# Performance work log

Measured on AMD Instinct MI355X. Metric: run time of the kernel, lower is better.

## Reference

```python
import jax, jax.numpy as jnp
import numpy as np

D_MODEL = 256

def setup_inputs() -> dict:
    key = jax.random.key(0)
    k_x, k_wqkv, k_bqkv, k_wp, k_bp = jax.random.split(key, 5)
    B, T, d = 4, 4096, D_MODEL
    bound_qkv = 1.0 / np.sqrt(d)
    return {
        "x": jax.random.normal(k_x, (B, T, d), dtype=jnp.float32),
        "W_qkv": jax.random.uniform(k_wqkv, (d, 3 * d), jnp.float32, -bound_qkv, bound_qkv),
        "b_qkv": jax.random.uniform(k_bqkv, (3 * d,), jnp.float32, -bound_qkv, bound_qkv),
        "W_proj": jax.random.uniform(k_wp, (d, d), jnp.float32, -bound_qkv, bound_qkv),
        "b_proj": jax.random.uniform(k_bp, (d,), jnp.float32, -bound_qkv, bound_qkv),
    }

def reference(x, W_qkv, b_qkv, W_proj, b_proj):
    B, T, d = x.shape
    qkv = x @ W_qkv + b_qkv                       # (B, T, 3d)
    q, k, v = jnp.split(qkv, 3, axis=-1)          # each (B, T, d)
    scale = 1.0 / np.sqrt(d).astype(np.float32)
    scores = jnp.einsum('btd,bsd->bts', q, k) * scale   # (B, T, T)
    causal = jnp.tril(jnp.ones((T, T), dtype=bool))     # allowed positions
    scores = jnp.where(causal, scores, -jnp.inf)
    weights = jax.nn.softmax(scores, axis=-1)           # (B, T, T)
    ctx = jnp.einsum('bts,bsd->btd', weights, v)        # (B, T, d)
    return ctx @ W_proj + b_proj
```

## Files before the change

### kernel.cpp

```cpp
#include <hip/hip_runtime.h>
#include <math.h>

#define TT 4096
#define BB 4
#define DM 256
#define NSEG_B 144

typedef __attribute__((ext_vector_type(8))) short short8;
typedef __attribute__((ext_vector_type(4))) short short4v;
typedef __attribute__((ext_vector_type(4))) float f32x4;

#define MFMA16(a, b, c) __builtin_amdgcn_mfma_f32_16x16x32_bf16(a, b, c, 0, 0, 0)

#define GL2LDS(gp, lp) __builtin_amdgcn_global_load_lds( \
    (const __attribute__((address_space(1))) unsigned int*)(gp), \
    (__attribute__((address_space(3))) unsigned int*)(lp), 16, 0, 0)

__device__ __forceinline__ short f2b(float f) {
    union { float f; unsigned u; } v; v.f = f;
    unsigned r = v.u + 0x7FFFu + ((v.u >> 16) & 1u);
    return (short)(r >> 16);
}

__global__ __launch_bounds__(256) void transpose_cast2(
    const float* __restrict__ W1, short* __restrict__ Wt1,
    const float* __restrict__ W2, short* __restrict__ Wt2)
{
    __shared__ float T[64 * 68];
    const int tid = threadIdx.x;
    const int by = blockIdx.y;
    const float* W; short* Wt; int N, n0;
    if (by < 12) { W = W1; Wt = Wt1; N = 768; n0 = by * 64; }
    else         { W = W2; Wt = Wt2; N = 256; n0 = (by - 12) * 64; }
    const int k0 = blockIdx.x * 64;
#pragma unroll
    for (int it = 0; it < 4; ++it) {
        int idx = tid + it * 256;
        int r = idx >> 4, c4 = idx & 15;
        *(float4*)&T[r * 68 + c4 * 4] =
            *(const float4*)&W[(size_t)(k0 + r) * N + n0 + c4 * 4];
    }
    __syncthreads();
#pragma unroll
    for (int it = 0; it < 4; ++it) {
        int idx = tid + it * 256;
        int n = idx >> 4, c4 = idx & 15;
        short4v t;
#pragma unroll
        for (int j = 0; j < 4; ++j) t[j] = f2b(T[(c4 * 4 + j) * 68 + n]);
        *(short4v*)&Wt[(size_t)(n0 + n) * 256 + k0 + c4 * 4] = t;
    }
}

__global__ __launch_bounds__(256) void qkv_gemm(
    const float* __restrict__ x, const short* __restrict__ Bt,
    const float* __restrict__ bias, short* __restrict__ qkvb,
    short* __restrict__ VtG)
{
    __shared__ short As[16384];
    __shared__ short Bs[16384];
    __shared__ short Ts[64 * 72];

    const int tid = threadIdx.x;
    const int w = tid >> 6, lane = tid & 63;
    const int l15 = lane & 15, quad = lane >> 4;
    const int m0 = blockIdx.x * 64;
    const int nsup = blockIdx.y * 384;

#pragma unroll
    for (int it = 0; it < 8; ++it) {
        int idx = tid + it * 256;
        int row = ((idx >> 9) << 4) + (idx & 15);
        int col = ((idx >> 6) & 7) * 32 + ((idx >> 4) & 3) * 8;
        const float* src = &x[(size_t)(m0 + row) * 256 + col];
        float4 u = *(const float4*)src, u2 = *(const float4*)(src + 4);
        short8 t;
        t[0] = f2b(u.x);  t[1] = f2b(u.y);  t[2] = f2b(u.z);  t[3] = f2b(u.w);
        t[4] = f2b(u2.x); t[5] = f2b(u2.y); t[6] = f2b(u2.z); t[7] = f2b(u2.w);
        *(short8*)&As[idx * 8] = t;
    }

    for (int t6 = 0; t6 < 6; ++t6) {
        const int n0 = nsup + t6 * 64;
#pragma unroll
        for (int it = 0; it < 8; ++it) {
            int idx = tid + it * 256;
            int n = ((idx >> 9) << 4) + (idx & 15);
            int col = ((idx >> 6) & 7) * 32 + ((idx >> 4) & 3) * 8;
            *(short8*)&Bs[idx * 8] = *(const short8*)&Bt[(size_t)(n0 + n) * 256 + col];
        }
        __syncthreads();

        f32x4 acc[4];
#pragma unroll
        for (int t = 0; t < 4; ++t) acc[t] = (f32x4){0.f, 0.f, 0.f, 0.f};
#pragma unroll
        for (int k0 = 0; k0 < 8; ++k0) {
            short8 a = *(const short8*)&As[((w * 8 + k0) * 64 + lane) * 8];
#pragma unroll
            for (int nt = 0; nt < 4; ++nt) {
                short8 bb = *(const short8*)&Bs[((nt * 8 + k0) * 64 + lane) * 8];
                acc[nt] = MFMA16(a, bb, acc[nt]);
            }
        }

        if (n0 < 512) {
#pragma unroll
            for (int nt = 0; nt < 4; ++nt) {
                int n = n0 + nt * 16 + l15;
                float bv = bias[n];
#pragma unroll
                for (int r = 0; r < 4; ++r)
                    qkvb[(size_t)(m0 + w * 16 + quad * 4 + r) * 768 + n]
                        = f2b(acc[nt][r] + bv);
            }
            __syncthreads();
        } else {
#pragma unroll
            for (int nt = 0; nt < 4; ++nt) {
                int n = n0 + nt * 16 + l15;
                float bv = bias[n];
#pragma unroll
                for (int r = 0; r < 4; ++r)
                    Ts[(nt * 16 + l15) * 72 + w * 16 + quad * 4 + r]
                        = f2b(acc[nt][r] + bv);
            }
            __syncthreads();
            const int d  = tid >> 2;
            const int c  = tid & 3;
            short8 v0 = *(const short8*)&Ts[d * 72 + c * 16];
            short8 v1 = *(const short8*)&Ts[d * 72 + c * 16 + 8];
            const int bg = m0 >> 12, key0 = (m0 & 4095) + c * 16;
            short* dst = &VtG[((size_t)bg * 256 + (n0 - 512) + d) * 4096 + key0];
            *(short8*)dst = v0;
            *(short8*)(dst + 8) = v1;
        }
    }
}

__global__ __launch_bounds__(256, 2) void flash_mfma(
    const short* __restrict__ qkv,
    const short* __restrict__ VtG,
    float* __restrict__ Opart,
    float* __restrict__ L)
{
    __shared__ short Ks[2][8192];
    __shared__ short Vs[2][8192];
    __shared__ short Ps[4096];

    const int tid = threadIdx.x;
    const int w = tid >> 6, lane = tid & 63;
    const int l15 = lane & 15, quad = lane >> 4;

    const int b = blockIdx.x & 3;
    const int e = (NSEG_B - 1) - (blockIdx.x >> 2);
    const int lid = b * NSEG_B + e;
    int g = 0;
    while (g < 7 && e >= 2 * (g + 1) * (g + 2)) ++g;
    int off = e - 2 * g * (g + 1);
    int qt = 4 * g + off / (g + 1);
    int s  = off - (off / (g + 1)) * (g + 1);
    const int kb_lo = s * 16;
    const int kb_hi = min(kb_lo + 16, 4 * (qt + 1));
    const int nunits = kb_hi - kb_lo;

    const size_t base = (size_t)b * TT * 768;
    const int row0 = qt * 128;

    short8 aq[2][8];
#pragma unroll
    for (int rs = 0; rs < 2; ++rs) {
        const short* qrow = &qkv[base + (size_t)(row0 + rs * 64 + w * 16 + l15) * 768 + quad * 8];
#pragma unroll
        for (int k0 = 0; k0 < 8; ++k0)
            aq[rs][k0] = *(const short8*)&qrow[k0 * 32];
    }

#pragma unroll
    for (int it = 0; it < 4; ++it) {
        int idx = tid + it * 256;
        int row = ((idx >> 9) << 4) + (idx & 15);
        int col = ((idx >> 6) & 7) * 32 + ((idx >> 4) & 3) * 8;
        GL2LDS(&qkv[base + (size_t)(kb_lo * 32 + row) * 768 + 256 + col], &Ks[0][idx * 8]);
        int d  = ((idx >> 6) << 4) + (idx & 15);
        int kc = ((idx >> 4) & 3) * 8;
        GL2LDS(&VtG[((size_t)b * 256 + d) * 4096 + kb_lo * 32 + kc], &Vs[0][idx * 8]);
    }

    f32x4 o[2][16];
#pragma unroll
    for (int rs = 0; rs < 2; ++rs)
#pragma unroll
        for (int c = 0; c < 16; ++c) o[rs][c] = (f32x4){0.f, 0.f, 0.f, 0.f};
    float l_acc[2][4] = {{0.f, 0.f, 0.f, 0.f}, {0.f, 0.f, 0.f, 0.f}};

    for (int u = 0; u < nunits; ++u) {
        const int p = u & 1;
        const int j0 = (kb_lo + u) * 32;

        __syncthreads();

        if (u + 1 < nunits) {
            const int j0n = j0 + 32;
#pragma unroll
            for (int it = 0; it < 4; ++it) {
                int idx = tid + it * 256;
                int row = ((idx >> 9) << 4) + (idx & 15);
                int col = ((idx >> 6) & 7) * 32 + ((idx >> 4) & 3) * 8;
                GL2LDS(&qkv[base + (size_t)(j0n + row) * 768 + 256 + col], &Ks[p ^ 1][idx * 8]);
                int d  = ((idx >> 6) << 4) + (idx & 15);
                int kc = ((idx >> 4) & 3) * 8;
                GL2LDS(&VtG[((size_t)b * 256 + d) * 4096 + j0n + kc], &Vs[p ^ 1][idx * 8]);
            }
        }

        f32x4 s4[2][2];
#pragma unroll
        for (int rs = 0; rs < 2; ++rs)
#pragma unroll
            for (int nt = 0; nt < 2; ++nt) s4[rs][nt] = (f32x4){0.f, 0.f, 0.f, 0.f};
#pragma unroll
        for (int k0 = 0; k0 < 8; ++k0) {
#pragma unroll
            for (int nt = 0; nt < 2; ++nt) {
                short8 bb = *(const short8*)&Ks[p][((nt * 8 + k0) * 64 + lane) * 8];
                s4[0][nt] = MFMA16(aq[0][k0], bb, s4[0][nt]);
                s4[1][nt] = MFMA16(aq[1][k0], bb, s4[1][nt]);
            }
        }

#pragma unroll
        for (int rs = 0; rs < 2; ++rs) {
#pragma unroll
            for (int r = 0; r < 4; ++r) {
                const int rg = row0 + rs * 64 + w * 16 + quad * 4 + r;
#pragma unroll
                for (int nt = 0; nt < 2; ++nt) {
                    int jg = j0 + nt * 16 + l15;
                    float xx = s4[rs][nt][r] * 0.0625f;
                    if (jg > rg) xx = -INFINITY;
                    float pv = __expf(fminf(xx, 30.f));
                    l_acc[rs][r] += pv;
                    Ps[((rs * 4 + w) * 64 + (nt * 2 + (l15 >> 3)) * 16 + quad * 4 + r) * 8
                       + (l15 & 7)] = f2b(pv);
                }
            }
        }

        {
            short8 a0 = *(const short8*)&Ps[((0 * 4 + w) * 64 + lane) * 8];
            short8 a1 = *(const short8*)&Ps[((1 * 4 + w) * 64 + lane) * 8];
#pragma unroll
            for (int ct = 0; ct < 16; ++ct) {
                short8 bb = *(const short8*)&Vs[p][(ct * 64 + lane) * 8];
                o[0][ct] = MFMA16(a0, bb, o[0][ct]);
                o[1][ct] = MFMA16(a1, bb, o[1][ct]);
            }
        }
    }

#pragma unroll
    for (int rs = 0; rs < 2; ++rs)
#pragma unroll
        for (int r = 0; r < 4; ++r) {
            float l = l_acc[rs][r];
            l += __shfl_xor(l, 1); l += __shfl_xor(l, 2);
            l += __shfl_xor(l, 4); l += __shfl_xor(l, 8);
            if (l15 == 0)
                L[(size_t)lid * 128 + rs * 64 + w * 16 + quad * 4 + r] = l;
        }
    const size_t ob = (size_t)lid * (128 * 256);
#pragma unroll
    for (int rs = 0; rs < 2; ++rs)
#pragma unroll
        for (int r = 0; r < 4; ++r) {
            int lr = rs * 64 + w * 16 + quad * 4 + r;
#pragma unroll
            for (int c = 0; c < 16; ++c)
                Opart[ob + (size_t)lr * 256 + c * 16 + l15] = o[rs][c][r];
        }
}

__global__ __launch_bounds__(256) void proj_gemm(
    const float* __restrict__ Opart, const float* __restrict__ L,
    const short* __restrict__ Bt, const float* __restrict__ bias,
    float* __restrict__ out)
{
    __shared__ short As[16384];
    __shared__ short Bs[16384];
    __shared__ float Linv[64];

    const int tid = threadIdx.x;
    const int w = tid >> 6, lane = tid & 63;
    const int l15 = lane & 15, quad = lane >> 4;
    const int t = blockIdx.x;
    const int b = t >> 6, q64 = t & 63;
    const int qt = q64 >> 1, half = q64 & 1;
    const int gg = qt >> 2, rr = qt & 3;
    const int sbase = b * NSEG_B + 2 * gg * (gg + 1) + rr * (gg + 1);
    const int nseg = gg + 1;
    const int m0 = t * 64;
    const int ro = half * 64;

    if (tid < 64) {
        float l = 0.f;
#pragma unroll
        for (int s2 = 0; s2 < 8; ++s2)
            if (s2 < nseg) l += L[(size_t)(sbase + s2) * 128 + ro + tid];
        Linv[tid] = 1.f / l;
    }
    __syncthreads();

#pragma unroll
    for (int it = 0; it < 8; ++it) {
        int idx = tid + it * 256;
        int row = ((idx >> 9) << 4) + (idx & 15);
        int col = ((idx >> 6) & 7) * 32 + ((idx >> 4) & 3) * 8;
        float a8[8] = {0.f, 0.f, 0.f, 0.f, 0.f, 0.f, 0.f, 0.f};
#pragma unroll
        for (int s2 = 0; s2 < 8; ++s2) {
            if (s2 < nseg) {
                const float* src = &Opart[(size_t)(sbase + s2) * 32768
                                          + (size_t)(ro + row) * 256 + col];
                float4 u = *(const float4*)src, u2 = *(const float4*)(src + 4);
                a8[0] += u.x;  a8[1] += u.y;  a8[2] += u.z;  a8[3] += u.w;
                a8[4] += u2.x; a8[5] += u2.y; a8[6] += u2.z; a8[7] += u2.w;
            }
        }
        float inv = Linv[row];
        short8 t8;
#pragma unroll
        for (int j = 0; j < 8; ++j) t8[j] = f2b(a8[j] * inv);
        *(short8*)&As[idx * 8] = t8;
    }

    for (int t2 = 0; t2 < 2; ++t2) {
        const int n0 = blockIdx.y * 128 + t2 * 64;
#pragma unroll
        for (int it = 0; it < 8; ++it) {
            int idx = tid + it * 256;
            int n = ((idx >> 9) << 4) + (idx & 15);
            int col = ((idx >> 6) & 7) * 32 + ((idx >> 4) & 3) * 8;
            *(short8*)&Bs[idx * 8] = *(const short8*)&Bt[(size_t)(n0 + n) * 256 + col];
        }
        __syncthreads();

        f32x4 acc[4];
#pragma unroll
        for (int tt = 0; tt < 4; ++tt) acc[tt] = (f32x4){0.f, 0.f, 0.f, 0.f};
#pragma unroll
        for (int k0 = 0; k0 < 8; ++k0) {
            short8 a = *(const short8*)&As[((w * 8 + k0) * 64 + lane) * 8];
#pragma unroll
            for (int nt = 0; nt < 4; ++nt) {
                short8 bb = *(const short8*)&Bs[((nt * 8 + k0) * 64 + lane) * 8];
                acc[nt] = MFMA16(a, bb, acc[nt]);
            }
        }
#pragma unroll
        for (int nt = 0; nt < 4; ++nt) {
            int n = n0 + nt * 16 + l15;
            float bv = bias[n];
#pragma unroll
            for (int r = 0; r < 4; ++r)
                out[(size_t)(m0 + w * 16 + quad * 4 + r) * 256 + n] = acc[nt][r] + bv;
        }
        __syncthreads();
    }
}

extern "C" void kernel_launch(void* const* d_in, const int* in_sizes, int n_in,
                              void* d_out, int out_size, void* d_ws, size_t ws_size,
                              hipStream_t stream)
{
    const float* x     = (const float*)d_in[0];
    const float* Wqkv  = (const float*)d_in[1];
    const float* bqkv  = (const float*)d_in[2];
    const float* Wproj = (const float*)d_in[3];
    const float* bproj = (const float*)d_in[4];
    float* out = (float*)d_out;

    const size_t M = (size_t)BB * TT;
    short* qkv_b = (short*)d_ws;
    short* Wt1   = qkv_b + M * 768;
    short* Wt2   = Wt1 + (size_t)768 * 256;
    short* VtG   = Wt2 + (size_t)256 * 256;
    float* Opart = (float*)(VtG + (size_t)BB * 256 * 4096);
    float* L     = Opart + (size_t)BB * NSEG_B * 128 * 256;

    dim3 blk(256);
    transpose_cast2<<<dim3(4, 16), blk, 0, stream>>>(Wqkv, Wt1, Wproj, Wt2);
    qkv_gemm<<<dim3(256, 2), blk, 0, stream>>>(x, Wt1, bqkv, qkv_b, VtG);
    flash_mfma<<<dim3(BB * NSEG_B), blk, 0, stream>>>(qkv_b, VtG, Opart, L);
    proj_gemm<<<dim3(256, 2), blk, 0, stream>>>(Opart, L, Wt2, bproj, out);
}
```

Measured before the change: 240.8 us.

## Shrink flash query tile to 64 rows and double segment count for occupancy

The flash kernel's query tile drops from 128 to 64 rows per block, so there are twice as many segments (288 per batch). Accumulator registers and LDS use shrink, which allows 3 blocks per CU. The K tile is now staged in 16-key halves with an added barrier inside each iteration. The proj kernel reduction indexing changes to match. The trade-off is that K/V tiles are reused across fewer query rows, which raises global and LDS traffic per FLOP, and the extra synchronisation adds overhead.

```diff
diff --git a/kernel.cpp b/kernel.cpp
--- a/kernel.cpp
+++ b/kernel.cpp
@@ -4,7 +4,7 @@
 #define TT 4096
 #define BB 4
 #define DM 256
-#define NSEG_B 144
+#define NSEG_B 288
 
 typedef __attribute__((ext_vector_type(8))) short short8;
 typedef __attribute__((ext_vector_type(4))) short short4v;
@@ -138,15 +138,15 @@
     }
 }
 
-__global__ __launch_bounds__(256, 2) void flash_mfma(
+__global__ __launch_bounds__(256, 3) void flash_mfma(
     const short* __restrict__ qkv,
     const short* __restrict__ VtG,
     float* __restrict__ Opart,
     float* __restrict__ L)
 {
-    __shared__ short Ks[2][8192];
+    __shared__ short Ks[2][4096];
     __shared__ short Vs[2][8192];
-    __shared__ short Ps[4096];
+    __shared__ short Ps[2048];
 
     const int tid = threadIdx.x;
     const int w = tid >> 6, lane = tid & 63;
@@ -156,129 +156,144 @@
     const int e = (NSEG_B - 1) - (blockIdx.x >> 2);
     const int lid = b * NSEG_B + e;
     int g = 0;
-    while (g < 7 && e >= 2 * (g + 1) * (g + 2)) ++g;
-    int off = e - 2 * g * (g + 1);
-    int qt = 4 * g + off / (g + 1);
+    while (g < 7 && e >= 4 * (g + 1) * (g + 2)) ++g;
+    int off = e - 4 * g * (g + 1);
+    int qt = 8 * g + off / (g + 1);
     int s  = off - (off / (g + 1)) * (g + 1);
-    const int kb_lo = s * 16;
-    const int kb_hi = min(kb_lo + 16, 4 * (qt + 1));
-    const int nunits = kb_hi - kb_lo;
+    const int kp_lo = s * 16;
+    const int kp_hi = min(kp_lo + 16, 2 * (qt + 1));
+    const int npairs = kp_hi - kp_lo;
 
     const size_t base = (size_t)b * TT * 768;
-    const int row0 = qt * 128;
-
-    short8 aq[2][8];
-#pragma unroll
-    for (int rs = 0; rs < 2; ++rs) {
-        const short* qrow = &qkv[base + (size_t)(row0 + rs * 64 + w * 16 + l15) * 768 + quad * 8];
+    const int row0 = qt * 64;
+
+    short8 aq[8];
+    {
+        const short* qrow = &qkv[base + (size_t)(row0 + w * 16 + l15) * 768 + quad * 8];
 #pragma unroll
         for (int k0 = 0; k0 < 8; ++k0)
-            aq[rs][k0] = *(const short8*)&qrow[k0 * 32];
-    }
-
+            aq[k0] = *(const short8*)&qrow[k0 * 32];
+    }
+
+#pragma unroll
+    for (int it = 0; it < 2; ++it) {
+        int idx = tid + it * 256;
+        int row = idx & 15;
+        int col = ((idx >> 6) & 7) * 32 + ((idx >> 4) & 3) * 8;
+        GL2LDS(&qkv[base + (size_t)(kp_lo * 32 + row) * 768 + 256 + col], &Ks[0][idx * 8]);
+    }
 #pragma unroll
     for (int it = 0; it < 4; ++it) {
         int idx = tid + it * 256;
-        int row = ((idx >> 9) << 4) + (idx & 15);
-        int col = ((idx >> 6) & 7) * 32 + ((idx >> 4) & 3) * 8;
-        GL2LDS(&qkv[base + (size_t)(kb_lo * 32 + row) * 768 + 256 + col], &Ks[0][idx * 8]);
         int d  = ((idx >> 6) << 4) + (idx & 15);
         int kc = ((idx >> 4) & 3) * 8;
-        GL2LDS(&VtG[((size_t)b * 256 + d) * 4096 + kb_lo * 32 + kc], &Vs[0][idx * 8]);
-    }
-
-    f32x4 o[2][16];
-#pragma unroll
-    for (int rs = 0; rs < 2; ++rs)
-#pragma unroll
-        for (int c = 0; c < 16; ++c) o[rs][c] = (f32x4){0.f, 0.f, 0.f, 0.f};
-    float l_acc[2][4] = {{0.f, 0.f, 0.f, 0.f}, {0.f, 0.f, 0.f, 0.f}};
-
-    for (int u = 0; u < nunits; ++u) {
-        const int p = u & 1;
-        const int j0 = (kb_lo + u) * 32;
+        GL2LDS(&VtG[((size_t)b * 256 + d) * 4096 + kp_lo * 32 + kc], &Vs[0][idx * 8]);
+    }
+
+    f32x4 o[16];
+#pragma unroll
+    for (int c = 0; c < 16; ++c) o[c] = (f32x4){0.f, 0.f, 0.f, 0.f};
+    float l_acc[4] = {0.f, 0.f, 0.f, 0.f};
+
+    for (int u = 0; u < npairs; ++u) {
+        const int j0 = (kp_lo + u) * 32;
 
         __syncthreads();
 
-        if (u + 1 < nunits) {
-            const int j0n = j0 + 32;
+#pragma unroll
+        for (int it = 0; it < 2; ++it) {
+            int idx = tid + it * 256;
+            int row = idx & 15;
+            int col = ((idx >> 6) & 7) * 32 + ((idx >> 4) & 3) * 8;
+            GL2LDS(&qkv[base + (size_t)(j0 + 16 + row) * 768 + 256 + col], &Ks[1][idx * 8]);
+        }
+        if (u + 1 < npairs) {
 #pragma unroll
             for (int it = 0; it < 4; ++it) {
                 int idx = tid + it * 256;
-                int row = ((idx >> 9) << 4) + (idx & 15);
-                int col = ((idx >> 6) & 7) * 32 + ((idx >> 4) & 3) * 8;
-                GL2LDS(&qkv[base + (size_t)(j0n + row) * 768 + 256 + col], &Ks[p ^ 1][idx * 8]);
                 int d  = ((idx >> 6) << 4) + (idx & 15);
                 int kc = ((idx >> 4) & 3) * 8;
-                GL2LDS(&VtG[((size_t)b * 256 + d) * 4096 + j0n + kc], &Vs[p ^ 1][idx * 8]);
-            }
-        }
-
-        f32x4 s4[2][2];
-#pragma unroll
-        for (int rs = 0; rs < 2; ++rs)
-#pragma unroll
-            for (int nt = 0; nt < 2; ++nt) s4[rs][nt] = (f32x4){0.f, 0.f, 0.f, 0.f};
-#pragma unroll
-        for (int k0 = 0; k0 < 8; ++k0) {
-#pragma unroll
-            for (int nt = 0; nt < 2; ++nt) {
-                short8 bb = *(const short8*)&Ks[p][((nt * 8 + k0) * 64 + lane) * 8];
-                s4[0][nt] = MFMA16(aq[0][k0], bb, s4[0][nt]);
-                s4[1][nt] = MFMA16(aq[1][k0], bb, s4[1][nt]);
-            }
-        }
-
-#pragma unroll
-        for (int rs = 0; rs < 2; ++rs) {
+                GL2LDS(&VtG[((size_t)b * 256 + d) * 4096 + j0 + 32 + kc],
+                       &Vs[(u + 1) & 1][idx * 8]);
+            }
+        }
+
+        {
+            f32x4 s4 = (f32x4){0.f, 0.f, 0.f, 0.f};
+#pragma unroll
+            for (int k0 = 0; k0 < 8; ++k0) {
+                short8 bb = *(const short8*)&Ks[0][(k0 * 64 + lane) * 8];
+                s4 = MFMA16(aq[k0], bb, s4);
+            }
 #pragma unroll
             for (int r = 0; r < 4; ++r) {
-                const int rg = row0 + rs * 64 + w * 16 + quad * 4 + r;
-#pragma unroll
-                for (int nt = 0; nt < 2; ++nt) {
-                    int jg = j0 + nt * 16 + l15;
-                    float xx = s4[rs][nt][r] * 0.0625f;
-                    if (jg > rg) xx = -INFINITY;
-                    float pv = __expf(fminf(xx, 30.f));
-                    l_acc[rs][r] += pv;
-                    Ps[((rs * 4 + w) * 64 + (nt * 2 + (l15 >> 3)) * 16 + quad * 4 + r) * 8
-                       + (l15 & 7)] = f2b(pv);
-                }
+                const int rg = row0 + w * 16 + quad * 4 + r;
+                int jg = j0 + l15;
+                float xx = s4[r] * 0.0625f;
+                if (jg > rg) xx = -INFINITY;
+                float pv = __expf(fminf(xx, 30.f));
+                l_acc[r] += pv;
+                Ps[(w * 64 + (l15 >> 3) * 16 + quad * 4 + r) * 8 + (l15 & 7)] = f2b(pv);
+            }
+        }
+
+        __syncthreads();
+
+        if (u + 1 < npairs) {
+#pragma unroll
+            for (int it = 0; it < 2; ++it) {
+                int idx = tid + it * 256;
+                int row = idx & 15;
+                int col = ((idx >> 6) & 7) * 32 + ((idx >> 4) & 3) * 8;
+                GL2LDS(&qkv[base + (size_t)(j0 + 32 + row) * 768 + 256 + col], &Ks[0][idx * 8]);
             }
         }
 
         {
-            short8 a0 = *(const short8*)&Ps[((0 * 4 + w) * 64 + lane) * 8];
-            short8 a1 = *(const short8*)&Ps[((1 * 4 + w) * 64 + lane) * 8];
+            f32x4 s4 = (f32x4){0.f, 0.f, 0.f, 0.f};
+#pragma unroll
+            for (int k0 = 0; k0 < 8; ++k0) {
+                short8 bb = *(const short8*)&Ks[1][(k0 * 64 + lane) * 8];
+                s4 = MFMA16(aq[k0], bb, s4);
+            }
+#pragma unroll
+            for (int r = 0; r < 4; ++r) {
+                const int rg = row0 + w * 16 + quad * 4 + r;
+                int jg = j0 + 16 + l15;
+                float xx = s4[r] * 0.0625f;
+                if (jg > rg) xx = -INFINITY;
+                float pv = __expf(fminf(xx, 30.f));
+                l_acc[r] += pv;
+                Ps[(w * 64 + (2 + (l15 >> 3)) * 16 + quad * 4 + r) * 8 + (l15 & 7)] = f2b(pv);
+            }
+        }
+
+        {
+            short8 a0 = *(const short8*)&Ps[(w * 64 + lane) * 8];
 #pragma unroll
             for (int ct = 0; ct < 16; ++ct) {
-                short8 bb = *(const short8*)&Vs[p][(ct * 64 + lane) * 8];
-                o[0][ct] = MFMA16(a0, bb, o[0][ct]);
-                o[1][ct] = MFMA16(a1, bb, o[1][ct]);
-            }
-        }
-    }
-
-#pragma unroll
-    for (int rs = 0; rs < 2; ++rs)
-#pragma unroll
-        for (int r = 0; r < 4; ++r) {
-            float l = l_acc[rs][r];
-            l += __shfl_xor(l, 1); l += __shfl_xor(l, 2);
-            l += __shfl_xor(l, 4); l += __shfl_xor(l, 8);
-            if (l15 == 0)
-                L[(size_t)lid * 128 + rs * 64 + w * 16 + quad * 4 + r] = l;
-        }
-    const size_t ob = (size_t)lid * (128 * 256);
-#pragma unroll
-    for (int rs = 0; rs < 2; ++rs)
-#pragma unroll
-        for (int r = 0; r < 4; ++r) {
-            int lr = rs * 64 + w * 16 + quad * 4 + r;
-#pragma unroll
-            for (int c = 0; c < 16; ++c)
-                Opart[ob + (size_t)lr * 256 + c * 16 + l15] = o[rs][c][r];
-        }
+                short8 bb = *(const short8*)&Vs[u & 1][(ct * 64 + lane) * 8];
+                o[ct] = MFMA16(a0, bb, o[ct]);
+            }
+        }
+    }
+
+#pragma unroll
+    for (int r = 0; r < 4; ++r) {
+        float l = l_acc[r];
+        l += __shfl_xor(l, 1); l += __shfl_xor(l, 2);
+        l += __shfl_xor(l, 4); l += __shfl_xor(l, 8);
+        if (l15 == 0)
+            L[(size_t)lid * 64 + w * 16 + quad * 4 + r] = l;
+    }
+    const size_t ob = (size_t)lid * (64 * 256);
+#pragma unroll
+    for (int r = 0; r < 4; ++r) {
+        int lr = w * 16 + quad * 4 + r;
+#pragma unroll
+        for (int c = 0; c < 16; ++c)
+            Opart[ob + (size_t)lr * 256 + c * 16 + l15] = o[c][r];
+    }
 }
 
 __global__ __launch_bounds__(256) void proj_gemm(
@@ -294,19 +309,17 @@
     const int w = tid >> 6, lane = tid & 63;
     const int l15 = lane & 15, quad = lane >> 4;
     const int t = blockIdx.x;
-    const int b = t >> 6, q64 = t & 63;
-    const int qt = q64 >> 1, half = q64 & 1;
-    const int gg = qt >> 2, rr = qt & 3;
-    const int sbase = b * NSEG_B + 2 * gg * (gg + 1) + rr * (gg + 1);
+    const int b = t >> 6, qt = t & 63;
+    const int gg = qt >> 3, rr = qt & 7;
+    const int sbase = b * NSEG_B + 4 * gg * (gg + 1) + rr * (gg + 1);
     const int nseg = gg + 1;
     const int m0 = t * 64;
-    const int ro = half * 64;
 
     if (tid < 64) {
         float l = 0.f;
 #pragma unroll
         for (int s2 = 0; s2 < 8; ++s2)
-            if (s2 < nseg) l += L[(size_t)(sbase + s2) * 128 + ro + tid];
+            if (s2 < nseg) l += L[(size_t)(sbase + s2) * 64 + tid];
         Linv[tid] = 1.f / l;
     }
     __syncthreads();
@@ -320,8 +333,8 @@
 #pragma unroll
         for (int s2 = 0; s2 < 8; ++s2) {
             if (s2 < nseg) {
-                const float* src = &Opart[(size_t)(sbase + s2) * 32768
-                                          + (size_t)(ro + row) * 256 + col];
+                const float* src = &Opart[(size_t)(sbase + s2) * 16384
+                                          + (size_t)row * 256 + col];
                 float4 u = *(const float4*)src, u2 = *(const float4*)(src + 4);
                 a8[0] += u.x;  a8[1] += u.y;  a8[2] += u.z;  a8[3] += u.w;
                 a8[4] += u2.x; a8[5] += u2.y; a8[6] += u2.z; a8[7] += u2.w;
@@ -386,7 +399,7 @@
     short* Wt2   = Wt1 + (size_t)768 * 256;
     short* VtG   = Wt2 + (size_t)256 * 256;
     float* Opart = (float*)(VtG + (size_t)BB * 256 * 4096);
-    float* L     = Opart + (size_t)BB * NSEG_B * 128 * 256;
+    float* L     = Opart + (size_t)BB * NSEG_B * 64 * 256;
 
     dim3 blk(256);
     transpose_cast2<<<dim3(4, 16), blk, 0, stream>>>(Wqkv, Wt1, Wproj, Wt2);
```

New measurement: 226.6 us. 5.9% less time.

## Split K tile into half-tile stages and merge proj_gemm column blocks

Applied to the files above, without the earlier changes.

The flash kernel now stages K in 16-row halves through two small LDS buffers, with explicit vmcnt waits and barriers, so the second half-tile load overlaps the QK^T and softmax of the first half. V stays double-buffered per 32-key unit, and K's LDS footprint is halved. Separately, proj_gemm covers all 256 output columns in one block instead of splitting them across two blocks along y. This avoids re-reducing the partial O sums twice, but it halves the grid size.

```diff
diff --git a/kernel.cpp b/kernel.cpp
--- a/kernel.cpp
+++ b/kernel.cpp
@@ -144,7 +144,7 @@
     float* __restrict__ Opart,
     float* __restrict__ L)
 {
-    __shared__ short Ks[2][8192];
+    __shared__ short Ks[2][4096];
     __shared__ short Vs[2][8192];
     __shared__ short Ps[4096];
 
@@ -160,9 +160,9 @@
     int off = e - 2 * g * (g + 1);
     int qt = 4 * g + off / (g + 1);
     int s  = off - (off / (g + 1)) * (g + 1);
-    const int kb_lo = s * 16;
-    const int kb_hi = min(kb_lo + 16, 4 * (qt + 1));
-    const int nunits = kb_hi - kb_lo;
+    const int kp_lo = s * 16;
+    const int kp_hi = min(kp_lo + 16, 4 * (qt + 1));
+    const int npairs = kp_hi - kp_lo;
 
     const size_t base = (size_t)b * TT * 768;
     const int row0 = qt * 128;
@@ -177,14 +177,19 @@
     }
 
 #pragma unroll
+    for (int it = 0; it < 2; ++it) {
+        int idx = tid + it * 256;
+        int row = idx & 15;
+        int col = ((idx >> 6) & 7) * 32 + ((idx >> 4) & 3) * 8;
+        GL2LDS(&qkv[base + (size_t)(kp_lo * 32 + row) * 768 + 256 + col], &Ks[0][idx * 8]);
+    }
+    __builtin_amdgcn_sched_barrier(0);
+#pragma unroll
     for (int it = 0; it < 4; ++it) {
         int idx = tid + it * 256;
-        int row = ((idx >> 9) << 4) + (idx & 15);
-        int col = ((idx >> 6) & 7) * 32 + ((idx >> 4) & 3) * 8;
-        GL2LDS(&qkv[base + (size_t)(kb_lo * 32 + row) * 768 + 256 + col], &Ks[0][idx * 8]);
         int d  = ((idx >> 6) << 4) + (idx & 15);
         int kc = ((idx >> 4) & 3) * 8;
-        GL2LDS(&VtG[((size_t)b * 256 + d) * 4096 + kb_lo * 32 + kc], &Vs[0][idx * 8]);
+        GL2LDS(&VtG[((size_t)b * 256 + d) * 4096 + kp_lo * 32 + kc], &Vs[0][idx * 8]);
     }
 
     f32x4 o[2][16];
@@ -194,57 +199,98 @@
         for (int c = 0; c < 16; ++c) o[rs][c] = (f32x4){0.f, 0.f, 0.f, 0.f};
     float l_acc[2][4] = {{0.f, 0.f, 0.f, 0.f}, {0.f, 0.f, 0.f, 0.f}};
 
-    for (int u = 0; u < nunits; ++u) {
-        const int p = u & 1;
-        const int j0 = (kb_lo + u) * 32;
+    for (int u = 0; u < npairs; ++u) {
+        const int j0 = (kp_lo + u) * 32;
 
         __syncthreads();
 
-        if (u + 1 < nunits) {
-            const int j0n = j0 + 32;
+#pragma unroll
+        for (int it = 0; it < 2; ++it) {
+            int idx = tid + it * 256;
+            int row = idx & 15;
+            int col = ((idx >> 6) & 7) * 32 + ((idx >> 4) & 3) * 8;
+            GL2LDS(&qkv[base + (size_t)(j0 + 16 + row) * 768 + 256 + col], &Ks[1][idx * 8]);
+        }
+        __builtin_amdgcn_sched_barrier(0);
+        if (u + 1 < npairs) {
 #pragma unroll
             for (int it = 0; it < 4; ++it) {
                 int idx = tid + it * 256;
-                int row = ((idx >> 9) << 4) + (idx & 15);
-                int col = ((idx >> 6) & 7) * 32 + ((idx >> 4) & 3) * 8;
-                GL2LDS(&qkv[base + (size_t)(j0n + row) * 768 + 256 + col], &Ks[p ^ 1][idx * 8]);
                 int d  = ((idx >> 6) << 4) + (idx & 15);
                 int kc = ((idx >> 4) & 3) * 8;
-                GL2LDS(&VtG[((size_t)b * 256 + d) * 4096 + j0n + kc], &Vs[p ^ 1][idx * 8]);
-            }
-        }
-
-        f32x4 s4[2][2];
-#pragma unroll
-        for (int rs = 0; rs < 2; ++rs)
-#pragma unroll
-            for (int nt = 0; nt < 2; ++nt) s4[rs][nt] = (f32x4){0.f, 0.f, 0.f, 0.f};
-#pragma unroll
-        for (int k0 = 0; k0 < 8; ++k0) {
-#pragma unroll
-            for (int nt = 0; nt < 2; ++nt) {
-                short8 bb = *(const short8*)&Ks[p][((nt * 8 + k0) * 64 + lane) * 8];
-                s4[0][nt] = MFMA16(aq[0][k0], bb, s4[0][nt]);
-                s4[1][nt] = MFMA16(aq[1][k0], bb, s4[1][nt]);
-            }
-        }
-
-#pragma unroll
-        for (int rs = 0; rs < 2; ++rs) {
-#pragma unroll
-            for (int r = 0; r < 4; ++r) {
-                const int rg = row0 + rs * 64 + w * 16 + quad * 4 + r;
-#pragma unroll
-                for (int nt = 0; nt < 2; ++nt) {
-                    int jg = j0 + nt * 16 + l15;
-                    float xx = s4[rs][nt][r] * 0.0625f;
+                GL2LDS(&VtG[((size_t)b * 256 + d) * 4096 + j0 + 32 + kc],
+                       &Vs[(u + 1) & 1][idx * 8]);
+            }
+        }
+        __builtin_amdgcn_sched_barrier(0);
+
+        {
+            f32x4 s4[2];
+            s4[0] = (f32x4){0.f, 0.f, 0.f, 0.f};
+            s4[1] = (f32x4){0.f, 0.f, 0.f, 0.f};
+#pragma unroll
+            for (int k0 = 0; k0 < 8; ++k0) {
+                short8 bb = *(const short8*)&Ks[0][(k0 * 64 + lane) * 8];
+                s4[0] = MFMA16(aq[0][k0], bb, s4[0]);
+                s4[1] = MFMA16(aq[1][k0], bb, s4[1]);
+            }
+#pragma unroll
+            for (int rs = 0; rs < 2; ++rs)
+#pragma unroll
+                for (int r = 0; r < 4; ++r) {
+                    const int rg = row0 + rs * 64 + w * 16 + quad * 4 + r;
+                    int jg = j0 + l15;
+                    float xx = s4[rs][r] * 0.0625f;
                     if (jg > rg) xx = -INFINITY;
                     float pv = __expf(fminf(xx, 30.f));
                     l_acc[rs][r] += pv;
-                    Ps[((rs * 4 + w) * 64 + (nt * 2 + (l15 >> 3)) * 16 + quad * 4 + r) * 8
+                    Ps[((rs * 4 + w) * 64 + (0 * 2 + (l15 >> 3)) * 16 + quad * 4 + r) * 8
                        + (l15 & 7)] = f2b(pv);
                 }
-            }
+        }
+
+        if (u + 1 < npairs) {
+            asm volatile("s_waitcnt vmcnt(4)" ::: "memory");
+        } else {
+            asm volatile("s_waitcnt vmcnt(0)" ::: "memory");
+        }
+        __builtin_amdgcn_s_barrier();
+        __builtin_amdgcn_sched_barrier(0);
+
+        if (u + 1 < npairs) {
+#pragma unroll
+            for (int it = 0; it < 2; ++it) {
+                int idx = tid + it * 256;
+                int row = idx & 15;
+                int col = ((idx >> 6) & 7) * 32 + ((idx >> 4) & 3) * 8;
+                GL2LDS(&qkv[base + (size_t)(j0 + 32 + row) * 768 + 256 + col], &Ks[0][idx * 8]);
+            }
+        }
+        __builtin_amdgcn_sched_barrier(0);
+
+        {
+            f32x4 s4[2];
+            s4[0] = (f32x4){0.f, 0.f, 0.f, 0.f};
+            s4[1] = (f32x4){0.f, 0.f, 0.f, 0.f};
+#pragma unroll
+            for (int k0 = 0; k0 < 8; ++k0) {
+                short8 bb = *(const short8*)&Ks[1][(k0 * 64 + lane) * 8];
+                s4[0] = MFMA16(aq[0][k0], bb, s4[0]);
+                s4[1] = MFMA16(aq[1][k0], bb, s4[1]);
+            }
+#pragma unroll
+            for (int rs = 0; rs < 2; ++rs)
+#pragma unroll
+                for (int r = 0; r < 4; ++r) {
+                    const int rg = row0 + rs * 64 + w * 16 + quad * 4 + r;
+                    int jg = j0 + 16 + l15;
+                    float xx = s4[rs][r] * 0.0625f;
+                    if (jg > rg) xx = -INFINITY;
+                    float pv = __expf(fminf(xx, 30.f));
+                    l_acc[rs][r] += pv;
+                    Ps[((rs * 4 + w) * 64 + (1 * 2 + (l15 >> 3)) * 16 + quad * 4 + r) * 8
+                       + (l15 & 7)] = f2b(pv);
+                }
         }
 
         {
@@ -252,7 +298,7 @@
             short8 a1 = *(const short8*)&Ps[((1 * 4 + w) * 64 + lane) * 8];
 #pragma unroll
             for (int ct = 0; ct < 16; ++ct) {
-                short8 bb = *(const short8*)&Vs[p][(ct * 64 + lane) * 8];
+                short8 bb = *(const short8*)&Vs[u & 1][(ct * 64 + lane) * 8];
                 o[0][ct] = MFMA16(a0, bb, o[0][ct]);
                 o[1][ct] = MFMA16(a1, bb, o[1][ct]);
             }
@@ -334,8 +380,8 @@
         *(short8*)&As[idx * 8] = t8;
     }
 
-    for (int t2 = 0; t2 < 2; ++t2) {
-        const int n0 = blockIdx.y * 128 + t2 * 64;
+    for (int t2 = 0; t2 < 4; ++t2) {
+        const int n0 = t2 * 64;
 #pragma unroll
         for (int it = 0; it < 8; ++it) {
             int idx = tid + it * 256;
@@ -392,5 +438,5 @@
     transpose_cast2<<<dim3(4, 16), blk, 0, stream>>>(Wqkv, Wt1, Wproj, Wt2);
     qkv_gemm<<<dim3(256, 2), blk, 0, stream>>>(x, Wt1, bqkv, qkv_b, VtG);
     flash_mfma<<<dim3(BB * NSEG_B), blk, 0, stream>>>(qkv_b, VtG, Opart, L);
-    proj_gemm<<<dim3(256, 2), blk, 0, stream>>>(Opart, L, Wt2, bproj, out);
-}
+    proj_gemm<<<dim3(256), blk, 0, stream>>>(Opart, L, Wt2, bproj, out);
+}
```

After: 239.1 us. Within noise of the previous version (-0.7%).
